# Kernel tuning notes

Measured on AMD Instinct MI355X. Metric: run time of the kernel, lower is better.

Reference implementation:

```python
import jax, jax.numpy as jnp
import numpy as np

P_SIZE = 5
NUM_HEAD = 8
GN_EPS = 1e-5
LRELU_SLOPE = 0.2


def conv1x1(w, x, b=None):
    # w: [out_c, in_c], x: [n, in_c, h, w]
    y = jnp.einsum('oc,nchw->nohw', w, x)
    if b is not None:
        y = y + b[None, :, None, None]
    return y


def bilinear_sample(feat, sx, sy):
    """grid_sample(mode='bilinear', padding_mode='zeros', align_corners=True).
    With align_corners=True the normalize/denormalize round-trip in
    deformation_grid/grid_sample is the identity, so sx,sy are raw pixel coords.
    feat: [n,c,H,W]; sx,sy: [n,P,H,W] -> out [n,c,P,H,W]."""
    n, c, H, W = feat.shape
    x0 = jnp.floor(sx)
    y0 = jnp.floor(sy)
    x1 = x0 + 1.0
    y1 = y0 + 1.0
    wx1 = sx - x0
    wx0 = 1.0 - wx1
    wy1 = sy - y0
    wy0 = 1.0 - wy1
    feat_flat = feat.reshape(n, c, H * W)

    def corner(xi, yi, wgt):
        valid = (xi >= 0) & (xi <= W - 1) & (yi >= 0) & (yi <= H - 1)
        xc = jnp.clip(xi, 0, W - 1).astype(jnp.int32)
        yc = jnp.clip(yi, 0, H - 1).astype(jnp.int32)
        idx = (yc * W + xc).reshape(n, -1)                      # [n, P*H*W]
        g = jnp.take_along_axis(feat_flat, idx[:, None, :], axis=2)  # [n,c,P*H*W]
        g = g.reshape(n, c, xi.shape[1], H, W)                  # [n,c,P,H,W]
        wm = (wgt * valid.astype(feat.dtype))[:, None]          # [n,1,P,H,W]
        return g * wm

    return (corner(x0, y0, wx0 * wy0) + corner(x1, y0, wx1 * wy0)
            + corner(x0, y1, wx0 * wy1) + corner(x1, y1, wx1 * wy1))


def sample_coords(deform_field, p_size):
    # deform_field: [n,2,h,w] -> absolute pixel coords sx, sy: [n, p^2, h, w]
    n, _, h, w = deform_field.shape
    padding = (p_size - 1) // 2
    shift = jnp.arange(p_size, dtype=deform_field.dtype) - padding
    shift_y, shift_x = jnp.meshgrid(shift, shift, indexing='ij')  # [p,p]
    shift_y = shift_y.reshape(-1, 1, 1)  # [p^2,1,1]
    shift_x = shift_x.reshape(-1, 1, 1)
    gy = jnp.arange(h, dtype=deform_field.dtype)[:, None]  # [h,1]
    gx = jnp.arange(w, dtype=deform_field.dtype)[None, :]  # [1,w]
    sx = gx[None] + shift_x + deform_field[:, None, 0]     # [n,p^2,h,w]
    sy = gy[None] + shift_y + deform_field[:, None, 1]
    return sx, sy


def setup_inputs() -> dict:
    key = jax.random.key(0)
    ks = jax.random.split(key, 12)
    n, c, h, w = 2, 128, 96, 96
    hid = 256
    s = 0.05
    return {
        'query': jax.random.normal(ks[0], (n, c, h, w), jnp.float32),
        'key': jax.random.normal(ks[1], (n, c, h, w), jnp.float32),
        'value': jax.random.normal(ks[2], (n, c, h, w), jnp.float32),
        'deform_field': jax.random.normal(ks[3], (n, 2, h, w), jnp.float32) * 2.0,
        'w_q': jax.random.normal(ks[4], (c, c), jnp.float32) * s,
        'w_k': jax.random.normal(ks[5], (c, c), jnp.float32) * s,
        'w_v': jax.random.normal(ks[6], (c, c), jnp.float32) * s,
        'w_fc': jax.random.normal(ks[7], (c, c), jnp.float32) * s,
        'mlp_w1': jax.random.normal(ks[8], (hid, c), jnp.float32) * s,
        'mlp_b1': jnp.zeros((hid,), jnp.float32),
        'mlp_w2': jax.random.normal(ks[9], (c, hid), jnp.float32) * s,
        'mlp_b2': jnp.zeros((c,), jnp.float32),
        'gn_gamma': jnp.ones((c,), jnp.float32),
        'gn_beta': jnp.zeros((c,), jnp.float32),
    }


def reference(query, key, value, deform_field, w_q, w_k, w_v, w_fc,
              mlp_w1, mlp_b1, mlp_w2, mlp_b2, gn_gamma, gn_beta):
    p2 = P_SIZE * P_SIZE
    n, c, h, w = query.shape
    d_k = c // NUM_HEAD

    q = conv1x1(w_q, query)   # [n,c,h,w]
    k = conv1x1(w_k, key)
    v = conv1x1(w_v, value)

    # deformable window sampling of keys/values
    sx, sy = sample_coords(deform_field, P_SIZE)      # [n,p^2,h,w]
    k_s = bilinear_sample(k, sx, sy)                  # [n,c,p^2,h,w]
    v_s = bilinear_sample(v, sx, sy)

    # split heads
    q = q.reshape(n, NUM_HEAD, d_k, h, w)
    k_s = k_s.reshape(n, NUM_HEAD, d_k, p2, h, w)
    v_s = v_s.reshape(n, NUM_HEAD, d_k, p2, h, w)

    scale = 1.0 / jnp.sqrt(jnp.asarray(d_k, q.dtype))
    attn = jnp.einsum('nedyx,nedpyx->neyxp', q * scale, k_s)   # [n,head,h,w,p^2]
    attn = jax.nn.softmax(attn, axis=-1)
    out = jnp.einsum('neyxp,nedpyx->nedyx', attn, v_s)          # [n,head,d_v,h,w]
    out = out.reshape(n, c, h, w)
    out = conv1x1(w_fc, out)

    # conv-MLP residual
    hdn = conv1x1(mlp_w1, out, mlp_b1)
    hdn = jnp.where(hdn >= 0, hdn, LRELU_SLOPE * hdn)
    out = out + conv1x1(mlp_w2, hdn, mlp_b2)

    # GroupNorm(1, feat_dim): normalize over (C,H,W) per sample, per-channel affine
    mean = jnp.mean(out, axis=(1, 2, 3), keepdims=True)
    var = jnp.mean(jnp.square(out - mean), axis=(1, 2, 3), keepdims=True)
    out = (out - mean) * jax.lax.rsqrt(var + GN_EPS)
    out = out * gn_gamma[None, :, None, None] + gn_beta[None, :, None, None]
    return out
```

## Files before the change

### kernel.cpp

```cpp
#include <hip/hip_runtime.h>
#include <cstddef>

constexpr int Cc = 128;
constexpr int Hh = 96;
constexpr int Ww = 96;
constexpr int HW = Hh * Ww;
constexpr int Nn = 2;

typedef __attribute__((ext_vector_type(2))) _Float16 f16x2;
typedef __attribute__((ext_vector_type(4))) _Float16 f16x4;
typedef __attribute__((ext_vector_type(8))) _Float16 f16x8;
typedef __attribute__((ext_vector_type(4))) float f32x4;

__device__ __forceinline__ float fdot2(f16x2 a, f16x2 b, float c) {
#if defined(__has_builtin) && __has_builtin(__builtin_amdgcn_fdot2)
    return __builtin_amdgcn_fdot2(a, b, c, false);
#else
    return (float)a[0] * (float)b[0] + (float)a[1] * (float)b[1] + c;
#endif
}

__global__ void __launch_bounds__(256)
wcvt_k(const float* __restrict__ wq, const float* __restrict__ wk,
       const float* __restrict__ wv, const float* __restrict__ wfc,
       const float* __restrict__ w1, const float* __restrict__ w2,
       _Float16* __restrict__ dst)
{
    const int h0 = (blockIdx.x * 256 + threadIdx.x) * 8;
    const float* src; int off, K;
    if (h0 < 16384)      { src = wq;  off = h0;          K = 128; }
    else if (h0 < 32768) { src = wk;  off = h0 - 16384;  K = 128; }
    else if (h0 < 49152) { src = wv;  off = h0 - 32768;  K = 128; }
    else if (h0 < 65536) { src = wfc; off = h0 - 49152;  K = 128; }
    else if (h0 < 98304) { src = w1;  off = h0 - 65536;  K = 128; }
    else                 { src = w2;  off = h0 - 98304;  K = 256; }
    const int fid  = off >> 3;
    const int lane = fid & 63;
    const int n16  = lane & 15, quad = lane >> 4;
    const int t2   = fid >> 6;
    const int kcN  = K / 32;
    const int kc   = t2 % kcN;
    const int mt   = t2 / kcN;
    const int row  = mt * 16 + n16;
    const int col  = kc * 32 + quad * 8;
    const float* s = src + (size_t)row * K + col;
    const float4 a = *(const float4*)s;
    const float4 b = *(const float4*)(s + 4);
    f16x8 h = {(_Float16)a.x, (_Float16)a.y, (_Float16)a.z, (_Float16)a.w,
               (_Float16)b.x, (_Float16)b.y, (_Float16)b.z, (_Float16)b.w};
    *(f16x8*)&dst[h0] = h;
}

__global__ void __launch_bounds__(128)
qkv_k(const float* __restrict__ Xq, const float* __restrict__ Xk,
      const float* __restrict__ Xv, const _Float16* __restrict__ w16,
      _Float16* __restrict__ q16, _Float16* __restrict__ k16,
      _Float16* __restrict__ v16)
{
    const int t  = blockIdx.y;
    const int p0 = blockIdx.x * 64;
    const int z  = blockIdx.z;
    const float* X = (t == 0) ? Xq : (t == 1) ? Xk : Xv;
    _Float16* Y    = (t == 0) ? q16 : (t == 1) ? k16 : v16;
    const _Float16* W = w16 + (size_t)t * 16384;

    __shared__ _Float16 xl[128][72];
    const int tid = threadIdx.x;
    {
        const int px4 = (tid & 15) * 4, kg = tid >> 4;
        const float* Xz = X + (size_t)z * Cc * HW + p0 + px4;
#pragma unroll
        for (int kk = 0; kk < 16; ++kk) {
            const int k = kk * 8 + kg;
            float4 a = *(const float4*)&Xz[(size_t)k * HW];
            f16x4 h = {(_Float16)a.x, (_Float16)a.y, (_Float16)a.z, (_Float16)a.w};
            *(f16x4*)&xl[k][px4] = h;
        }
    }
    __syncthreads();

    const int w = tid >> 6, lane = tid & 63;
    const int n16 = lane & 15, quad = lane >> 4;
    const int pw = w * 32;

    f16x8 A[2][4];
#pragma unroll
    for (int mi = 0; mi < 2; ++mi) {
        const int px = pw + mi * 16 + n16;
#pragma unroll
        for (int kcid = 0; kcid < 4; ++kcid) {
            f16x8 av;
#pragma unroll
            for (int j = 0; j < 8; ++j) av[j] = xl[kcid * 32 + quad * 8 + j][px];
            A[mi][kcid] = av;
        }
    }

#pragma unroll
    for (int half = 0; half < 2; ++half) {
        const int oc0 = half * 64;
        f32x4 acc[2][4];
#pragma unroll
        for (int mi = 0; mi < 2; ++mi)
#pragma unroll
            for (int ni = 0; ni < 4; ++ni) acc[mi][ni] = (f32x4)0.f;

#pragma unroll
        for (int kcid = 0; kcid < 4; ++kcid) {
            f16x8 B[4];
#pragma unroll
            for (int ni = 0; ni < 4; ++ni)
                B[ni] = *(const f16x8*)&W[(((half * 4 + ni) * 4 + kcid) * 64 + lane) * 8];
#pragma unroll
            for (int mi = 0; mi < 2; ++mi)
#pragma unroll
                for (int ni = 0; ni < 4; ++ni)
                    acc[mi][ni] = __builtin_amdgcn_mfma_f32_16x16x32_f16(
                        A[mi][kcid], B[ni], acc[mi][ni], 0, 0, 0);
        }

#pragma unroll
        for (int mi = 0; mi < 2; ++mi)
#pragma unroll
            for (int r = 0; r < 4; ++r) {
                const int pix = p0 + pw + mi * 16 + quad * 4 + r;
                const size_t base = ((size_t)z * HW + pix) * Cc + oc0;
#pragma unroll
                for (int ni = 0; ni < 4; ++ni)
                    Y[base + ni * 16 + n16] = (_Float16)acc[mi][ni][r];
            }
    }
}

template<int KT, bool OUTF16, bool BIAS, bool LRELU, bool RESID, bool REDUCE>
__global__ void __launch_bounds__(128)
mg_k(const _Float16* __restrict__ X, const _Float16* __restrict__ Wf,
     const float* __restrict__ bias, const _Float16* __restrict__ resid,
     void* __restrict__ Yv, float* __restrict__ pb, const int Mtot)
{
    constexpr int kcN = KT / 32;
    const int z = blockIdx.z, oc0 = blockIdx.y * 64, p0 = blockIdx.x * 64;
    const int tid = threadIdx.x, w = tid >> 6, lane = tid & 63;
    const int n16 = lane & 15, quad = lane >> 4;
    const _Float16* Xz = X + ((size_t)z * HW + p0 + w * 32) * KT;

    f32x4 acc[2][4];
#pragma unroll
    for (int mi = 0; mi < 2; ++mi)
#pragma unroll
        for (int ni = 0; ni < 4; ++ni) acc[mi][ni] = (f32x4)0.f;

#pragma unroll
    for (int kc = 0; kc < kcN; ++kc) {
        f16x8 A[2], B[4];
#pragma unroll
        for (int mi = 0; mi < 2; ++mi)
            A[mi] = *(const f16x8*)&Xz[(size_t)(mi * 16 + n16) * KT + kc * 32 + quad * 8];
#pragma unroll
        for (int ni = 0; ni < 4; ++ni)
            B[ni] = *(const f16x8*)&Wf[(((blockIdx.y * 4 + ni) * kcN + kc) * 64 + lane) * 8];
#pragma unroll
        for (int mi = 0; mi < 2; ++mi)
#pragma unroll
            for (int ni = 0; ni < 4; ++ni)
                acc[mi][ni] = __builtin_amdgcn_mfma_f32_16x16x32_f16(
                    A[mi], B[ni], acc[mi][ni], 0, 0, 0);
    }

    float bv[4];
#pragma unroll
    for (int ni = 0; ni < 4; ++ni) bv[ni] = BIAS ? bias[oc0 + ni * 16 + n16] : 0.f;

    float lsum = 0.f, lsq = 0.f;
#pragma unroll
    for (int mi = 0; mi < 2; ++mi)
#pragma unroll
        for (int r = 0; r < 4; ++r) {
            const int pix = p0 + w * 32 + mi * 16 + quad * 4 + r;
            const size_t ob = ((size_t)z * HW + pix) * (size_t)Mtot + oc0;
            const size_t rb = ((size_t)z * HW + pix) * 128 + oc0;
#pragma unroll
            for (int ni = 0; ni < 4; ++ni) {
                float tv = acc[mi][ni][r] + bv[ni];
                if (LRELU) tv = tv >= 0.f ? tv : 0.2f * tv;
                if (RESID) tv += (float)resid[rb + ni * 16 + n16];
                if (REDUCE) { lsum += tv; lsq += tv * tv; }
                if (OUTF16) ((_Float16*)Yv)[ob + ni * 16 + n16] = (_Float16)tv;
                else        ((float*)Yv)[ob + ni * 16 + n16] = tv;
            }
        }

    if (REDUCE) {
        __shared__ float red[4];
#pragma unroll
        for (int m = 1; m < 64; m <<= 1) {
            lsum += __shfl_xor(lsum, m, 64);
            lsq  += __shfl_xor(lsq,  m, 64);
        }
        if (lane == 0) { red[w * 2] = lsum; red[w * 2 + 1] = lsq; }
        __syncthreads();
        if (tid == 0) {
            const int bid = (blockIdx.z * gridDim.y + blockIdx.y) * gridDim.x + blockIdx.x;
            pb[bid * 2 + 0] = red[0] + red[2];
            pb[bid * 2 + 1] = red[1] + red[3];
        }
    }
}

__global__ void __launch_bounds__(256)
attn_k(const _Float16* __restrict__ q, const _Float16* __restrict__ k,
       const _Float16* __restrict__ v, const float* __restrict__ df,
       _Float16* __restrict__ out)
{
    const int blk = blockIdx.x;
    const int sw = (blk & 7) * (1152 / 8) + (blk >> 3);
    const int wv = sw * 4 + (threadIdx.x >> 6);
    const int lane = threadIdx.x & 63;
    const int gp = wv * 4 + (lane >> 4);
    const int b = gp / HW;
    const int pix = gp - b * HW;
    const int y = pix / Ww, x = pix - y * Ww;
    const int co = (lane & 15) * 8;

    const float dx = df[((size_t)b * 2 + 0) * HW + pix];
    const float dy = df[((size_t)b * 2 + 1) * HW + pix];
    const float flx = floorf(dx), fly = floorf(dy);
    const int bx = x - 2 + (int)flx;
    const int by = y - 2 + (int)fly;
    const float wx1 = dx - flx, wx0 = 1.f - wx1;
    const float wy1 = dy - fly, wy0 = 1.f - wy1;
    const float u00 = wy0 * wx0, u01 = wy0 * wx1, u10 = wy1 * wx0, u11 = wy1 * wx1;
    const float s00 = u00 * 0.25f, s01 = u01 * 0.25f,
                s10 = u10 * 0.25f, s11 = u11 * 0.25f;

    const f16x8 qv8 = *(const f16x8*)&q[((size_t)b * HW + pix) * Cc + co];
    const f16x2 q0 = {qv8[0], qv8[1]}, q1 = {qv8[2], qv8[3]},
                q2 = {qv8[4], qv8[5]}, q3 = {qv8[6], qv8[7]};

    const _Float16* kp = k + ((size_t)b * HW) * Cc + co;
    const _Float16* vp = v + ((size_t)b * HW) * Cc + co;

    const bool inb = (bx >= 0) & (by >= 0) & (bx <= Ww - 6) & (by <= Hh - 6);
    const int allin = __all(inb);

    float qk[36];
    if (allin) {
        const _Float16* kr = kp + (size_t)(by * Ww + bx) * Cc;
#pragma unroll
        for (int r = 0; r < 6; ++r) {
#pragma unroll
            for (int c = 0; c < 6; ++c) {
                const f16x8 kv = *(const f16x8*)&kr[c * Cc];
                f16x2 k0 = {kv[0], kv[1]}, k1 = {kv[2], kv[3]};
                f16x2 k2 = {kv[4], kv[5]}, k3 = {kv[6], kv[7]};
                float d = fdot2(q0, k0, 0.f);
                d = fdot2(q1, k1, d);
                d = fdot2(q2, k2, d);
                d = fdot2(q3, k3, d);
                qk[r * 6 + c] = d;
            }
            kr += Ww * Cc;
        }
    } else {
#pragma unroll
        for (int r = 0; r < 6; ++r) {
            const int yr = by + r;
            const bool rv = (yr >= 0) & (yr < Hh);
            const int yc = min(max(yr, 0), Hh - 1);
            const _Float16* kr = kp + (size_t)(yc * Ww) * Cc;
#pragma unroll
            for (int c = 0; c < 6; ++c) {
                const int xc = bx + c;
                const bool cv = rv & (xc >= 0) & (xc < Ww);
                const int xcc = min(max(xc, 0), Ww - 1);
                const f16x8 kv = *(const f16x8*)&kr[xcc * Cc];
                f16x2 k0 = {kv[0], kv[1]}, k1 = {kv[2], kv[3]};
                f16x2 k2 = {kv[4], kv[5]}, k3 = {kv[6], kv[7]};
                float d = fdot2(q0, k0, 0.f);
                d = fdot2(q1, k1, d);
                d = fdot2(q2, k2, d);
                d = fdot2(q3, k3, d);
                qk[r * 6 + c] = cv ? d : 0.f;
            }
        }
    }

    float a[25];
#pragma unroll
    for (int py = 0; py < 5; ++py)
#pragma unroll
        for (int px = 0; px < 5; ++px) {
            float tv = s00 * qk[py * 6 + px];
            tv = fmaf(s01, qk[py * 6 + px + 1], tv);
            tv = fmaf(s10, qk[(py + 1) * 6 + px], tv);
            tv = fmaf(s11, qk[(py + 1) * 6 + px + 1], tv);
            a[py * 5 + px] = tv;
        }
#pragma unroll
    for (int i = 0; i < 25; ++i) a[i] += __shfl_xor(a[i], 1, 64);

    float mx = a[0];
#pragma unroll
    for (int i = 1; i < 25; ++i) mx = fmaxf(mx, a[i]);
    float ssum = 0.f;
#pragma unroll
    for (int i = 0; i < 25; ++i) { a[i] = __expf(a[i] - mx); ssum += a[i]; }
    const float inv = 1.f / ssum;

    float tmp[6][5];
#pragma unroll
    for (int r = 0; r < 6; ++r)
#pragma unroll
        for (int px = 0; px < 5; ++px) {
            float tv = 0.f;
            if (r < 5)  tv = a[r * 5 + px] * wy0;
            if (r >= 1) tv = fmaf(a[(r - 1) * 5 + px], wy1, tv);
            tmp[r][px] = tv;
        }
    float wsum[36];
#pragma unroll
    for (int r = 0; r < 6; ++r)
#pragma unroll
        for (int c = 0; c < 6; ++c) {
            float tv = 0.f;
            if (c < 5)  tv = tmp[r][c] * wx0;
            if (c >= 1) tv = fmaf(tmp[r][c - 1], wx1, tv);
            wsum[r * 6 + c] = tv;
        }

    float o[8] = {0.f, 0.f, 0.f, 0.f, 0.f, 0.f, 0.f, 0.f};
    if (allin) {
        const _Float16* vr = vp + (size_t)(by * Ww + bx) * Cc;
#pragma unroll
        for (int r = 0; r < 6; ++r) {
#pragma unroll
            for (int c = 0; c < 6; ++c) {
                const f16x8 vv = *(const f16x8*)&vr[c * Cc];
                const float wgt = wsum[r * 6 + c];
#pragma unroll
                for (int j = 0; j < 8; ++j)
                    o[j] = fmaf(wgt, (float)vv[j], o[j]);
            }
            vr += Ww * Cc;
        }
    } else {
#pragma unroll
        for (int r = 0; r < 6; ++r) {
            const int yr = by + r;
            const bool rv = (yr >= 0) & (yr < Hh);
            const int yc = min(max(yr, 0), Hh - 1);
            const _Float16* vr = vp + (size_t)(yc * Ww) * Cc;
#pragma unroll
            for (int c = 0; c < 6; ++c) {
                const int xc = bx + c;
                const bool cv = rv & (xc >= 0) & (xc < Ww);
                const int xcc = min(max(xc, 0), Ww - 1);
                const f16x8 vv = *(const f16x8*)&vr[xcc * Cc];
                const float wgt = cv ? wsum[r * 6 + c] : 0.f;
#pragma unroll
                for (int j = 0; j < 8; ++j)
                    o[j] = fmaf(wgt, (float)vv[j], o[j]);
            }
        }
    }

    f16x8 ov;
#pragma unroll
    for (int j = 0; j < 8; ++j) ov[j] = (_Float16)(o[j] * inv);
    *(f16x8*)&out[((size_t)b * HW + pix) * Cc + co] = ov;
}

__global__ void __launch_bounds__(256)
gn_k(const float* __restrict__ y2, const float* __restrict__ pb,
     const float* __restrict__ gamma, const float* __restrict__ beta,
     float* __restrict__ out, const int nPerZ)
{
    __shared__ float t[32][68];
    __shared__ float redm[8];
    __shared__ float stats[2];
    const int z = blockIdx.z, c0 = blockIdx.y * 32, p0 = blockIdx.x * 64;
    const int tid = threadIdx.x;

    {
        float s = 0.f, qq = 0.f;
        for (int p = tid; p < nPerZ; p += 256) {
            s  += pb[(z * nPerZ + p) * 2 + 0];
            qq += pb[(z * nPerZ + p) * 2 + 1];
        }
#pragma unroll
        for (int m = 1; m < 64; m <<= 1) {
            s  += __shfl_xor(s,  m, 64);
            qq += __shfl_xor(qq, m, 64);
        }
        if ((tid & 63) == 0) {
            redm[(tid >> 6) * 2]     = s;
            redm[(tid >> 6) * 2 + 1] = qq;
        }
    }
    {
        const int px = tid >> 2, cq = tid & 3;
        const float* src = &y2[((size_t)z * HW + p0 + px) * Cc + c0 + cq * 8];
        const float4 a = *(const float4*)src;
        const float4 bq = *(const float4*)(src + 4);
        t[cq * 8 + 0][px] = a.x;  t[cq * 8 + 1][px] = a.y;
        t[cq * 8 + 2][px] = a.z;  t[cq * 8 + 3][px] = a.w;
        t[cq * 8 + 4][px] = bq.x; t[cq * 8 + 5][px] = bq.y;
        t[cq * 8 + 6][px] = bq.z; t[cq * 8 + 7][px] = bq.w;
    }
    __syncthreads();
    if (tid == 0) {
        const float invN = 1.f / (float)(Cc * HW);
        const float S = redm[0] + redm[2] + redm[4] + redm[6];
        const float Q = redm[1] + redm[3] + redm[5] + redm[7];
        const float mean = S * invN;
        const float var  = fmaf(-mean, mean, Q * invN);
        stats[0] = mean;
        stats[1] = rsqrtf(var + 1e-5f);
    }
    __syncthreads();
    {
        const float mean = stats[0], rs = stats[1];
        const int c = tid >> 3, pq = tid & 7;
        const float g = gamma[c0 + c] * rs, be = beta[c0 + c];
        float4 o1, o2;
        o1.x = fmaf(t[c][pq * 8 + 0] - mean, g, be);
        o1.y = fmaf(t[c][pq * 8 + 1] - mean, g, be);
        o1.z = fmaf(t[c][pq * 8 + 2] - mean, g, be);
        o1.w = fmaf(t[c][pq * 8 + 3] - mean, g, be);
        o2.x = fmaf(t[c][pq * 8 + 4] - mean, g, be);
        o2.y = fmaf(t[c][pq * 8 + 5] - mean, g, be);
        o2.z = fmaf(t[c][pq * 8 + 6] - mean, g, be);
        o2.w = fmaf(t[c][pq * 8 + 7] - mean, g, be);
        float* dst = &out[((size_t)z * Cc + c0 + c) * HW + p0 + pq * 8];
        *(float4*)dst = o1;
        *(float4*)(dst + 4) = o2;
    }
}

extern "C" void kernel_launch(void* const* d_in, const int* in_sizes, int n_in,
                              void* d_out, int out_size, void* d_ws, size_t ws_size,
                              hipStream_t stream)
{
    const float* query  = (const float*)d_in[0];
    const float* key    = (const float*)d_in[1];
    const float* value  = (const float*)d_in[2];
    const float* deform = (const float*)d_in[3];
    const float* w_q    = (const float*)d_in[4];
    const float* w_k    = (const float*)d_in[5];
    const float* w_v    = (const float*)d_in[6];
    const float* w_fc   = (const float*)d_in[7];
    const float* mlp_w1 = (const float*)d_in[8];
    const float* mlp_b1 = (const float*)d_in[9];
    const float* mlp_w2 = (const float*)d_in[10];
    const float* mlp_b2 = (const float*)d_in[11];
    const float* gn_g   = (const float*)d_in[12];
    const float* gn_b   = (const float*)d_in[13];
    float* out = (float*)d_out;

    char* wsb = (char*)d_ws;
    _Float16* w16 = (_Float16*)wsb;
    float* pb   = (float*)(wsb + 262144);
    _Float16* T = (_Float16*)(wsb + 524288);
    const size_t S16 = (size_t)Nn * HW * Cc;
    _Float16* q16  = T;
    _Float16* k16  = T + S16;
    _Float16* v16  = T + 2 * S16;
    _Float16* at16 = T + 3 * S16;
    _Float16* y1   = T + 4 * S16;
    _Float16* hb   = T;
    float*    y2   = (float*)(T + 2 * S16);

    wcvt_k<<<dim3(64), dim3(256), 0, stream>>>(
        w_q, w_k, w_v, w_fc, mlp_w1, mlp_w2, w16);

    qkv_k<<<dim3(HW / 64, 3, Nn), dim3(128), 0, stream>>>(
        query, key, value, w16, q16, k16, v16);

    attn_k<<<dim3(Nn * HW / 16), dim3(256), 0, stream>>>(
        q16, k16, v16, deform, at16);

    mg_k<128, true, false, false, false, false>
        <<<dim3(HW / 64, 2, Nn), dim3(128), 0, stream>>>(
        at16, w16 + 49152, nullptr, nullptr, y1, nullptr, 128);

    mg_k<128, true, true, true, false, false>
        <<<dim3(HW / 64, 4, Nn), dim3(128), 0, stream>>>(
        y1, w16 + 65536, mlp_b1, nullptr, hb, nullptr, 256);

    mg_k<256, false, true, false, true, true>
        <<<dim3(HW / 64, 2, Nn), dim3(128), 0, stream>>>(
        hb, w16 + 98304, mlp_b2, y1, y2, pb, 128);

    gn_k<<<dim3(HW / 64, Cc / 32, Nn), dim3(256), 0, stream>>>(
        y2, pb, gn_g, gn_b, out, 288);
}
```

Baseline: 156.2 us.

## Fuse fc projection and conv-MLP GEMMs into one LDS-staged kernel

Replaces the three separate GEMM launches (fc projection, MLP up-projection with bias and leaky ReLU, MLP down-projection with residual and GroupNorm partial sums) with a single kernel. Each block handles 32 pixels across all channels and keeps the intermediate y1 and hidden activations in shared memory instead of writing them to global memory. The residual is taken directly from the first accumulators. This removes the global round-trips for the intermediates and two launches, at the cost of larger per-block register and LDS use and a smaller pixel tile per block.

Measured after the change: 150.0 us. 1.04x faster.

```diff
diff --git a/kernel.cpp b/kernel.cpp
--- a/kernel.cpp
+++ b/kernel.cpp
@@ -132,81 +132,6 @@
     }
 }
 
-template<int KT, bool OUTF16, bool BIAS, bool LRELU, bool RESID, bool REDUCE>
-__global__ void __launch_bounds__(128)
-mg_k(const _Float16* __restrict__ X, const _Float16* __restrict__ Wf,
-     const float* __restrict__ bias, const _Float16* __restrict__ resid,
-     void* __restrict__ Yv, float* __restrict__ pb, const int Mtot)
-{
-    constexpr int kcN = KT / 32;
-    const int z = blockIdx.z, oc0 = blockIdx.y * 64, p0 = blockIdx.x * 64;
-    const int tid = threadIdx.x, w = tid >> 6, lane = tid & 63;
-    const int n16 = lane & 15, quad = lane >> 4;
-    const _Float16* Xz = X + ((size_t)z * HW + p0 + w * 32) * KT;
-
-    f32x4 acc[2][4];
-#pragma unroll
-    for (int mi = 0; mi < 2; ++mi)
-#pragma unroll
-        for (int ni = 0; ni < 4; ++ni) acc[mi][ni] = (f32x4)0.f;
-
-#pragma unroll
-    for (int kc = 0; kc < kcN; ++kc) {
-        f16x8 A[2], B[4];
-#pragma unroll
-        for (int mi = 0; mi < 2; ++mi)
-            A[mi] = *(const f16x8*)&Xz[(size_t)(mi * 16 + n16) * KT + kc * 32 + quad * 8];
-#pragma unroll
-        for (int ni = 0; ni < 4; ++ni)
-            B[ni] = *(const f16x8*)&Wf[(((blockIdx.y * 4 + ni) * kcN + kc) * 64 + lane) * 8];
-#pragma unroll
-        for (int mi = 0; mi < 2; ++mi)
-#pragma unroll
-            for (int ni = 0; ni < 4; ++ni)
-                acc[mi][ni] = __builtin_amdgcn_mfma_f32_16x16x32_f16(
-                    A[mi], B[ni], acc[mi][ni], 0, 0, 0);
-    }
-
-    float bv[4];
-#pragma unroll
-    for (int ni = 0; ni < 4; ++ni) bv[ni] = BIAS ? bias[oc0 + ni * 16 + n16] : 0.f;
-
-    float lsum = 0.f, lsq = 0.f;
-#pragma unroll
-    for (int mi = 0; mi < 2; ++mi)
-#pragma unroll
-        for (int r = 0; r < 4; ++r) {
-            const int pix = p0 + w * 32 + mi * 16 + quad * 4 + r;
-            const size_t ob = ((size_t)z * HW + pix) * (size_t)Mtot + oc0;
-            const size_t rb = ((size_t)z * HW + pix) * 128 + oc0;
-#pragma unroll
-            for (int ni = 0; ni < 4; ++ni) {
-                float tv = acc[mi][ni][r] + bv[ni];
-                if (LRELU) tv = tv >= 0.f ? tv : 0.2f * tv;
-                if (RESID) tv += (float)resid[rb + ni * 16 + n16];
-                if (REDUCE) { lsum += tv; lsq += tv * tv; }
-                if (OUTF16) ((_Float16*)Yv)[ob + ni * 16 + n16] = (_Float16)tv;
-                else        ((float*)Yv)[ob + ni * 16 + n16] = tv;
-            }
-        }
-
-    if (REDUCE) {
-        __shared__ float red[4];
-#pragma unroll
-        for (int m = 1; m < 64; m <<= 1) {
-            lsum += __shfl_xor(lsum, m, 64);
-            lsq  += __shfl_xor(lsq,  m, 64);
-        }
-        if (lane == 0) { red[w * 2] = lsum; red[w * 2 + 1] = lsq; }
-        __syncthreads();
-        if (tid == 0) {
-            const int bid = (blockIdx.z * gridDim.y + blockIdx.y) * gridDim.x + blockIdx.x;
-            pb[bid * 2 + 0] = red[0] + red[2];
-            pb[bid * 2 + 1] = red[1] + red[3];
-        }
-    }
-}
-
 __global__ void __launch_bounds__(256)
 attn_k(const _Float16* __restrict__ q, const _Float16* __restrict__ k,
        const _Float16* __restrict__ v, const float* __restrict__ df,
@@ -368,6 +293,150 @@
 #pragma unroll
     for (int j = 0; j < 8; ++j) ov[j] = (_Float16)(o[j] * inv);
     *(f16x8*)&out[((size_t)b * HW + pix) * Cc + co] = ov;
+}
+
+__global__ void __launch_bounds__(128)
+fmlp_k(const _Float16* __restrict__ X, const _Float16* __restrict__ w16,
+       const float* __restrict__ b1, const float* __restrict__ b2,
+       float* __restrict__ y2, float* __restrict__ pb)
+{
+    __shared__ __align__(16) _Float16 y1l[32][136];
+    __shared__ __align__(16) _Float16 hl[32][264];
+    __shared__ float red[4];
+
+    const int z  = blockIdx.z;
+    const int p0 = blockIdx.x * 32;
+    const int tid = threadIdx.x, w = tid >> 6, lane = tid & 63;
+    const int n16 = lane & 15, quad = lane >> 4;
+    const _Float16* Wfc = w16 + 49152;
+    const _Float16* W1  = w16 + 65536;
+    const _Float16* W2  = w16 + 98304;
+
+    f32x4 acc1[2][4];
+#pragma unroll
+    for (int mi = 0; mi < 2; ++mi)
+#pragma unroll
+        for (int ni = 0; ni < 4; ++ni) acc1[mi][ni] = (f32x4)0.f;
+
+    const _Float16* Xz = X + ((size_t)z * HW + p0) * 128;
+#pragma unroll
+    for (int kc = 0; kc < 4; ++kc) {
+        f16x8 A[2], B[4];
+#pragma unroll
+        for (int mi = 0; mi < 2; ++mi)
+            A[mi] = *(const f16x8*)&Xz[(size_t)(mi * 16 + n16) * 128 + kc * 32 + quad * 8];
+#pragma unroll
+        for (int ni = 0; ni < 4; ++ni)
+            B[ni] = *(const f16x8*)&Wfc[(((w * 4 + ni) * 4 + kc) * 64 + lane) * 8];
+#pragma unroll
+        for (int mi = 0; mi < 2; ++mi)
+#pragma unroll
+            for (int ni = 0; ni < 4; ++ni)
+                acc1[mi][ni] = __builtin_amdgcn_mfma_f32_16x16x32_f16(
+                    A[mi], B[ni], acc1[mi][ni], 0, 0, 0);
+    }
+#pragma unroll
+    for (int mi = 0; mi < 2; ++mi)
+#pragma unroll
+        for (int ni = 0; ni < 4; ++ni)
+#pragma unroll
+            for (int r = 0; r < 4; ++r)
+                y1l[mi * 16 + quad * 4 + r][w * 64 + ni * 16 + n16] =
+                    (_Float16)acc1[mi][ni][r];
+    __syncthreads();
+
+    f32x4 acc2[2][8];
+#pragma unroll
+    for (int mi = 0; mi < 2; ++mi)
+#pragma unroll
+        for (int ni = 0; ni < 8; ++ni) acc2[mi][ni] = (f32x4)0.f;
+
+#pragma unroll
+    for (int kc = 0; kc < 4; ++kc) {
+        f16x8 A[2];
+#pragma unroll
+        for (int mi = 0; mi < 2; ++mi)
+            A[mi] = *(const f16x8*)&y1l[mi * 16 + n16][kc * 32 + quad * 8];
+#pragma unroll
+        for (int ni = 0; ni < 8; ++ni) {
+            const f16x8 B = *(const f16x8*)&W1[(((w * 8 + ni) * 4 + kc) * 64 + lane) * 8];
+#pragma unroll
+            for (int mi = 0; mi < 2; ++mi)
+                acc2[mi][ni] = __builtin_amdgcn_mfma_f32_16x16x32_f16(
+                    A[mi], B, acc2[mi][ni], 0, 0, 0);
+        }
+    }
+    {
+        float b1v[8];
+#pragma unroll
+        for (int ni = 0; ni < 8; ++ni) b1v[ni] = b1[w * 128 + ni * 16 + n16];
+#pragma unroll
+        for (int mi = 0; mi < 2; ++mi)
+#pragma unroll
+            for (int ni = 0; ni < 8; ++ni)
+#pragma unroll
+                for (int r = 0; r < 4; ++r) {
+                    float tv = acc2[mi][ni][r] + b1v[ni];
+                    tv = tv >= 0.f ? tv : 0.2f * tv;
+                    hl[mi * 16 + quad * 4 + r][w * 128 + ni * 16 + n16] = (_Float16)tv;
+                }
+    }
+    __syncthreads();
+
+    f32x4 acc3[2][4];
+#pragma unroll
+    for (int mi = 0; mi < 2; ++mi)
+#pragma unroll
+        for (int ni = 0; ni < 4; ++ni) acc3[mi][ni] = (f32x4)0.f;
+
+#pragma unroll
+    for (int kc = 0; kc < 8; ++kc) {
+        f16x8 A[2], B[4];
+#pragma unroll
+        for (int mi = 0; mi < 2; ++mi)
+            A[mi] = *(const f16x8*)&hl[mi * 16 + n16][kc * 32 + quad * 8];
+#pragma unroll
+        for (int ni = 0; ni < 4; ++ni)
+            B[ni] = *(const f16x8*)&W2[(((w * 4 + ni) * 8 + kc) * 64 + lane) * 8];
+#pragma unroll
+        for (int mi = 0; mi < 2; ++mi)
+#pragma unroll
+            for (int ni = 0; ni < 4; ++ni)
+                acc3[mi][ni] = __builtin_amdgcn_mfma_f32_16x16x32_f16(
+                    A[mi], B[ni], acc3[mi][ni], 0, 0, 0);
+    }
+
+    float b2v[4];
+#pragma unroll
+    for (int ni = 0; ni < 4; ++ni) b2v[ni] = b2[w * 64 + ni * 16 + n16];
+
+    float lsum = 0.f, lsq = 0.f;
+#pragma unroll
+    for (int mi = 0; mi < 2; ++mi)
+#pragma unroll
+        for (int r = 0; r < 4; ++r) {
+            const int pix = p0 + mi * 16 + quad * 4 + r;
+            float* yp = &y2[((size_t)z * HW + pix) * 128 + w * 64];
+#pragma unroll
+            for (int ni = 0; ni < 4; ++ni) {
+                float tv = acc3[mi][ni][r] + b2v[ni] + acc1[mi][ni][r];
+                lsum += tv; lsq += tv * tv;
+                yp[ni * 16 + n16] = tv;
+            }
+        }
+
+#pragma unroll
+    for (int m = 1; m < 64; m <<= 1) {
+        lsum += __shfl_xor(lsum, m, 64);
+        lsq  += __shfl_xor(lsq,  m, 64);
+    }
+    if (lane == 0) { red[w * 2] = lsum; red[w * 2 + 1] = lsq; }
+    __syncthreads();
+    if (tid == 0) {
+        const int bid = blockIdx.z * gridDim.x + blockIdx.x;
+        pb[bid * 2 + 0] = red[0] + red[2];
+        pb[bid * 2 + 1] = red[1] + red[3];
+    }
 }
 
 __global__ void __launch_bounds__(256)
@@ -466,9 +535,7 @@
     _Float16* k16  = T + S16;
     _Float16* v16  = T + 2 * S16;
     _Float16* at16 = T + 3 * S16;
-    _Float16* y1   = T + 4 * S16;
-    _Float16* hb   = T;
-    float*    y2   = (float*)(T + 2 * S16);
+    float*    y2   = (float*)T;
 
     wcvt_k<<<dim3(64), dim3(256), 0, stream>>>(
         w_q, w_k, w_v, w_fc, mlp_w1, mlp_w2, w16);
@@ -479,18 +546,9 @@
     attn_k<<<dim3(Nn * HW / 16), dim3(256), 0, stream>>>(
         q16, k16, v16, deform, at16);
 
-    mg_k<128, true, false, false, false, false>
-        <<<dim3(HW / 64, 2, Nn), dim3(128), 0, stream>>>(
-        at16, w16 + 49152, nullptr, nullptr, y1, nullptr, 128);
-
-    mg_k<128, true, true, true, false, false>
-        <<<dim3(HW / 64, 4, Nn), dim3(128), 0, stream>>>(
-        y1, w16 + 65536, mlp_b1, nullptr, hb, nullptr, 256);
-
-    mg_k<256, false, true, false, true, true>
-        <<<dim3(HW / 64, 2, Nn), dim3(128), 0, stream>>>(
-        hb, w16 + 98304, mlp_b2, y1, y2, pb, 128);
+    fmlp_k<<<dim3(HW / 32, 1, Nn), dim3(128), 0, stream>>>(
+        at16, w16, mlp_b1, mlp_b2, y2, pb);
 
     gn_k<<<dim3(HW / 64, Cc / 32, Nn), dim3(256), 0, stream>>>(
-        y2, pb, gn_g, gn_b, out, 288);
-}
+        y2, pb, gn_g, gn_b, out, HW / 32);
+}
```
